# Kernel optimization log

Measured on AMD Instinct MI355X. Metric: run time of the kernel, lower is better.

Reference implementation:

```python
import jax, jax.numpy as jnp
import numpy as np

B, S, C, NH, DH, MH = 2, 2304, 1280, 8, 160, 64
SR = 48  # int(sqrt(S)); S = SR*SR
FMAX = jnp.finfo(jnp.float32).max


def _h2b(x):
    # diffusers head_to_batch_dim: [b,s,c] -> [b*heads, s, dh] (batch-major)
    b, s, c = x.shape
    return x.reshape(b, s, NH, DH).transpose(0, 2, 1, 3).reshape(b * NH, s, DH)


def _b2h(x):
    # diffusers batch_to_head_dim: [b*heads, s, dh] -> [b, s, c]
    bh, s, d = x.shape
    b = bh // NH
    return x.reshape(b, NH, s, d).transpose(0, 2, 1, 3).reshape(b, s, NH * d)


def _nearest(x, out):
    # torch F.interpolate(mode='nearest') on [b,1,h,w] square input -> [b,1,out,out]
    h, w = x.shape[-2], x.shape[-1]
    ih = jnp.arange(out) * h // out
    iw = jnp.arange(out) * w // out
    return x[:, :, ih, :][:, :, :, iw]


def setup_inputs():
    key = jax.random.key(0)
    ks = jax.random.split(key, 10)
    return {
        "hidden_states": jax.random.normal(ks[0], (B, S, C), jnp.float32),
        "Wq": jax.random.normal(ks[1], (C, C), jnp.float32) * 0.02,
        "Wk": jax.random.normal(ks[2], (C, C), jnp.float32) * 0.02,
        "Wv": jax.random.normal(ks[3], (C, C), jnp.float32) * 0.02,
        "Wo": jax.random.normal(ks[4], (C, C), jnp.float32) * 0.02,
        "bo": jnp.zeros((C,), jnp.float32),
        "store_ks": jax.random.normal(ks[5], (B * NH, S, DH), jnp.float32),
        "store_vs": jax.random.normal(ks[6], (B * NH, S, DH), jnp.float32),
        "mask_id": jax.random.bernoulli(ks[7], 0.5, (B, 1, MH, MH)),
        "mask_ig": jax.random.uniform(ks[8], (B, 1, MH, MH), jnp.float32),
        "scale_learnable": jnp.full((1,), 0.5, jnp.float32),
    }


def reference(hidden_states, Wq, Wk, Wv, Wo, bo, store_ks, store_vs, mask_id, mask_ig, scale_learnable):
    inv = 1.0 / jnp.sqrt(jnp.float32(DH))
    # self-attention (attention_mask is None for the self path)
    q = _h2b(hidden_states @ Wq)   # [B*NH, S, DH]
    k = _h2b(hidden_states @ Wk)
    v = _h2b(hidden_states @ Wv)
    probs = jax.nn.softmax(jnp.einsum('bqd,bkd->bqk', q, k) * inv, axis=-1)
    hs = _b2h(probs @ v)  # [B, S, C]
    # IP-adapter reference attention with interpolated additive mask
    mask_f = jnp.where(mask_id, jnp.float32(1.0), -FMAX)          # masked_fill(mask==False, -max)
    mask_r = _nearest(mask_f, SR).reshape(B, 1, SR * SR)          # [B,1,S], broadcast over query rows
    mask_bh = jnp.tile(mask_r, (NH, 1, 1))                        # torch .repeat(8,1,1) tiling order
    scores_ref = jnp.einsum('bqd,bkd->bqk', q, store_ks) * inv + mask_bh
    probs_ref = jax.nn.softmax(scores_ref, axis=-1)
    hs_ref = _b2h(probs_ref @ store_vs)                           # [B, S, C]
    # masked, learnable-scaled residual combine (self.scale = 1.0 python float)
    mask_ig_r = _nearest(mask_ig, SR).reshape(B, SR * SR, 1)      # 'b c h w -> b (h w) c'
    out = hs + 1.0 * hs_ref * mask_ig_r * scale_learnable
    # to_out[0] linear + to_out[1] dropout (identity at eval)
    return out @ Wo + bo
```

## Files before the change

### kernel.cpp

```cpp
#include <hip/hip_runtime.h>


typedef unsigned short u16;
typedef unsigned int   u32;
typedef unsigned char  u8;
typedef __attribute__((ext_vector_type(8))) short bf16x8;
typedef __attribute__((ext_vector_type(4))) float f32x4;

#define MFMA16(a,b,c) __builtin_amdgcn_mfma_f32_16x16x32_bf16((a),(b),(c),0,0,0)

__device__ __forceinline__ u16 f2b(float f) {
  u32 u = __float_as_uint(f);
  return (u16)((u + 0x7fffu + ((u >> 16) & 1u)) >> 16);
}
__device__ __forceinline__ float b2f(u16 v) { return __uint_as_float(((u32)v) << 16); }

__global__ __launch_bounds__(256) void maskdet(const u32* __restrict__ mid, u32* mode)
{
  __shared__ int a0, a1, a2, a3;
  int tid = threadIdx.x;
  if (tid == 0) { a0 = 1; a1 = 1; a2 = 1; a3 = 0; }
  __syncthreads();
  #pragma unroll
  for (int j = 0; j < 4; j++) {
    u32 w = mid[tid*4 + j];
    if (w > 1u)                      atomicAnd(&a0, 0);
    if (w & 0xFEFEFEFEu)             atomicAnd(&a1, 0);
    if (w != 0u && w != 0x3F800000u) atomicAnd(&a2, 0);
    if ((w & 0xFFFFu) == 0x3F80u)    atomicOr(&a3, 1);
  }
  __syncthreads();
  if (tid == 0) mode[0] = a0 ? 0u : (a1 ? 1u : (a3 ? 2u : (a2 ? 3u : 0u)));
}

__global__ void maskprep(const void* mid, const float* __restrict__ mig_in,
                         float* __restrict__ mk, float* __restrict__ mg, const u32* mode)
{
  int j = blockIdx.x*256 + threadIdx.x;
  if (j >= 2*2304) return;
  u32 md = mode[0];
  int b = j / 2304, s = j % 2304;
  int i = s / 48, jj = s % 48;
  int ih = (i*4)/3, iw = (jj*4)/3;
  int src = b*4096 + ih*64 + iw;
  bool on;
  if      (md == 0) on = ((const int*)mid)[src] != 0;
  else if (md == 1) on = ((const u8*)mid)[src]  != 0;
  else if (md == 2) on = ((const u16*)mid)[src] != 0;
  else              on = ((const float*)mid)[src] != 0.0f;
  mk[j] = on ? 1.0f : 0.0f;
  mg[j] = mig_in[src];
}

__global__ __launch_bounds__(256) void transpose_w(
    const float* __restrict__ W0, const float* __restrict__ W1,
    const float* __restrict__ W2, const float* __restrict__ W3, u16* __restrict__ WT)
{
  __shared__ u16 t[32][33];
  int z = blockIdx.z;
  const float* s = (z==0)?W0:(z==1)?W1:(z==2)?W2:W3;
  u16* d = WT + (size_t)z*1280*1280;
  int tx = threadIdx.x & 31, ty = (threadIdx.x >> 5) * 4;
  int x = blockIdx.x*32 + tx;
  int y = blockIdx.y*32 + ty;
  #pragma unroll
  for (int i=0;i<4;i++) t[ty+i][tx] = f2b(s[(size_t)(y+i)*1280 + x]);
  __syncthreads();
  int x2 = blockIdx.y*32 + tx, y2 = blockIdx.x*32 + ty;
  #pragma unroll
  for (int i=0;i<4;i++) d[(size_t)(y2+i)*1280 + x2] = t[tx][ty+i];
}

__global__ __launch_bounds__(256) void conv(const float* __restrict__ src, u16* __restrict__ dst, int n)
{
  for (int i = blockIdx.x*256 + threadIdx.x; i < n; i += gridDim.x*256)
    dst[i] = f2b(src[i]);
}

__global__ __launch_bounds__(256) void transpose_vs(const float* __restrict__ src, u16* __restrict__ dst)
{
  __shared__ u16 t[32][33];
  int z = blockIdx.z;
  u16* d = dst + (size_t)z*160*2304;
  int tx = threadIdx.x & 31, ty = (threadIdx.x >> 5) * 4;
  int r0 = blockIdx.x*32, c0 = blockIdx.y*32;
  #pragma unroll
  for (int i=0;i<4;i++)
    t[ty+i][tx] = f2b(src[((size_t)z*2304 + r0+ty+i)*160 + c0+tx]);
  __syncthreads();
  #pragma unroll
  for (int i=0;i<4;i++) d[(size_t)(c0+ty+i)*2304 + r0+tx] = t[tx][ty+i];
}

__global__ __launch_bounds__(256, 2) void gemm128(
    const u16* __restrict__ A, const u16* __restrict__ BT,
    u16* __restrict__ dq, u16* __restrict__ dk, u16* __restrict__ dvt,
    float* __restrict__ dout, const float* __restrict__ bias, int kind)
{
  __shared__ __align__(16) u16 As[128*40];
  __shared__ __align__(16) u16 Bs[128*40];
  int tid = threadIdx.x;
  int m0 = blockIdx.x*128, n0 = blockIdx.y*128;
  int z = blockIdx.z;
  const u16* Bt = BT + (size_t)z*1280*1280;
  int w = tid>>6, lane = tid&63, quad = lane>>4, l16 = lane&15;
  int wm = w&1, wn = w>>1;
  int arow = tid>>1, acg = (tid&1)*16;
  f32x4 zero = {0.f,0.f,0.f,0.f};
  f32x4 acc[4][4];
  #pragma unroll
  for (int a=0;a<4;a++) { acc[a][0]=zero; acc[a][1]=zero; acc[a][2]=zero; acc[a][3]=zero; }
  const u16* ga = A  + (size_t)(m0+arow)*1280 + acg;
  const u16* gb = Bt + (size_t)(n0+arow)*1280 + acg;
  for (int k0 = 0; k0 < 1280; k0 += 32) {
    uint4 a0 = *(const uint4*)(ga + k0);
    uint4 a1 = *(const uint4*)(ga + k0 + 8);
    uint4 b0 = *(const uint4*)(gb + k0);
    uint4 b1 = *(const uint4*)(gb + k0 + 8);
    __syncthreads();
    *(uint4*)&As[arow*40 + acg]     = a0;
    *(uint4*)&As[arow*40 + acg + 8] = a1;
    *(uint4*)&Bs[arow*40 + acg]     = b0;
    *(uint4*)&Bs[arow*40 + acg + 8] = b1;
    __syncthreads();
    bf16x8 af[4], bfr[4];
    #pragma unroll
    for (int mt=0; mt<4; mt++) af[mt]  = *(const bf16x8*)&As[(wm*64+mt*16+l16)*40 + quad*8];
    #pragma unroll
    for (int nt=0; nt<4; nt++) bfr[nt] = *(const bf16x8*)&Bs[(wn*64+nt*16+l16)*40 + quad*8];
    #pragma unroll
    for (int mt=0; mt<4; mt++)
      #pragma unroll
      for (int nt=0; nt<4; nt++)
        acc[mt][nt] = MFMA16(af[mt], bfr[nt], acc[mt][nt]);
  }
  #pragma unroll
  for (int mt=0; mt<4; mt++) {
    int r0g = m0 + wm*64 + mt*16 + quad*4;
    #pragma unroll
    for (int nt=0; nt<4; nt++) {
      int col = n0 + wn*64 + nt*16 + l16;
      if (kind == 1) {
        float bi = bias[col];
        #pragma unroll
        for (int r=0;r<4;r++) dout[(size_t)(r0g+r)*1280 + col] = acc[mt][nt][r] + bi;
      } else {
        int h = col/160, d = col%160;
        if (z == 2) {
          int b = r0g/2304, s0 = r0g%2304;
          size_t base = ((size_t)((b*8+h)*160 + d))*2304 + s0;
          ushort4 pk;
          pk.x = f2b(acc[mt][nt][0]); pk.y = f2b(acc[mt][nt][1]);
          pk.z = f2b(acc[mt][nt][2]); pk.w = f2b(acc[mt][nt][3]);
          *(ushort4*)&dvt[base] = pk;
        } else {
          u16* dst = (z==0)? dq : dk;
          #pragma unroll
          for (int r=0;r<4;r++) {
            int rg = r0g + r;
            int b = rg/2304, s = rg%2304;
            dst[((size_t)(b*8+h)*2304 + s)*160 + d] = f2b(acc[mt][nt][r]);
          }
        }
      }
    }
  }
}

__global__ __launch_bounds__(256, 2) void attn(
    const u16* __restrict__ qg,
    const u16* __restrict__ kg,
    const u16* __restrict__ vtg,
    const float* __restrict__ maskkey, const float* __restrict__ mig,
    u16* __restrict__ hs, u16* __restrict__ comb,
    const void* scaleptr, int ip)
{
  __shared__ __align__(16) u16 Ks[64*168];
  __shared__ __align__(16) u16 Ps[4*16*72];
  int bh = blockIdx.y, qt = blockIdx.x;
  int tid = threadIdx.x, w = tid>>6, lane = tid&63, quad = lane>>4, l16 = lane&15;
  int q0 = qt*64 + w*16;
  const float inv = 0.07905694150420949f;

  bf16x8 aq[5];
  {
    const u16* qrow = qg + ((size_t)bh*2304 + q0 + l16)*160 + quad*8;
    #pragma unroll
    for (int ks=0; ks<5; ks++) aq[ks] = *(const bf16x8*)(qrow + ks*32);
  }
  f32x4 zero = {0.f,0.f,0.f,0.f};
  f32x4 o[10];
  #pragma unroll
  for (int i=0;i<10;i++) o[i] = zero;
  float mrun[4] = {-1e30f,-1e30f,-1e30f,-1e30f};
  float lrun[4] = {0.f,0.f,0.f,0.f};

  int krow = tid>>2, kcg = (tid&3)*40;
  const u16* kbase = kg + ((size_t)bh*2304 + krow)*160 + kcg;
  const u16* vbase = vtg + ((size_t)bh*160 + l16)*2304 + quad*8;

  for (int kc = 0; kc < 36; kc++) {
    uint4 kv[5];
    #pragma unroll
    for (int i=0;i<5;i++) kv[i] = *(const uint4*)(kbase + (size_t)kc*64*160 + i*8);
    __syncthreads();
    #pragma unroll
    for (int i=0;i<5;i++) *(uint4*)&Ks[krow*168 + kcg + i*8] = kv[i];
    __syncthreads();

    f32x4 sc[4];
    bool keep[4];
    #pragma unroll
    for (int nt=0; nt<4; nt++) {
      f32x4 s = zero;
      #pragma unroll
      for (int ks=0; ks<5; ks++) {
        bf16x8 bk = *(const bf16x8*)&Ks[(nt*16+l16)*168 + ks*32 + quad*8];
        s = MFMA16(aq[ks], bk, s);
      }
      #pragma unroll
      for (int r=0;r<4;r++) s[r] *= inv;
      keep[nt] = true;
      if (ip) {
        int key = kc*64 + nt*16 + l16;
        if (maskkey[(bh & 1)*2304 + key] == 0.0f) {
          keep[nt] = false;
          #pragma unroll
          for (int r=0;r<4;r++) s[r] = -1e30f;
        }
      }
      sc[nt] = s;
    }

    float p[4][4];
    #pragma unroll
    for (int r=0;r<4;r++) {
      float mrow = fmaxf(fmaxf(sc[0][r], sc[1][r]), fmaxf(sc[2][r], sc[3][r]));
      #pragma unroll
      for (int off=1; off<16; off<<=1) mrow = fmaxf(mrow, __shfl_xor(mrow, off));
      float nm = fmaxf(mrun[r], mrow);
      float alpha = __expf(fminf(mrun[r] - nm, 0.f));
      mrun[r] = nm;
      float rs = 0.f;
      #pragma unroll
      for (int nt=0;nt<4;nt++) {
        float e = keep[nt] ? __expf(sc[nt][r] - nm) : 0.f;
        p[nt][r] = e; rs += e;
      }
      #pragma unroll
      for (int off=1; off<16; off<<=1) rs += __shfl_xor(rs, off);
      lrun[r] = lrun[r]*alpha + rs;
      #pragma unroll
      for (int nt2=0; nt2<10; nt2++) o[nt2][r] *= alpha;
    }

    #pragma unroll
    for (int nt=0;nt<4;nt++)
      #pragma unroll
      for (int r=0;r<4;r++)
        Ps[(w*16 + quad*4 + r)*72 + nt*16 + l16] = f2b(p[nt][r]);

    #pragma unroll
    for (int kb=0; kb<2; kb++) {
      bf16x8 ap = *(const bf16x8*)&Ps[(w*16 + l16)*72 + kb*32 + quad*8];
      #pragma unroll
      for (int nt=0; nt<10; nt++) {
        bf16x8 bv = *(const bf16x8*)(vbase + (size_t)nt*16*2304 + kc*64 + kb*32);
        o[nt] = MFMA16(ap, bv, o[nt]);
      }
    }
  }

  int b = bh>>3, h = bh&7;
  float scl = 0.f;
  if (ip) {
    u16 v0 = ((const u16*)scaleptr)[0];
    int e = (v0 >> 7) & 0xFF;
    scl = (v0 != 0 && e >= 100 && e <= 133) ? b2f(v0) : ((const float*)scaleptr)[0];
  }
  #pragma unroll
  for (int r=0;r<4;r++) {
    int s = q0 + quad*4 + r;
    float linv = (lrun[r] > 0.f) ? 1.0f/lrun[r] : 0.f;
    size_t base = ((size_t)b*2304 + s)*1280 + h*160;
    if (!ip) {
      #pragma unroll
      for (int nt=0;nt<10;nt++) hs[base + nt*16 + l16] = f2b(o[nt][r]*linv);
    } else {
      float f = mig[b*2304 + s]*scl*linv;
      #pragma unroll
      for (int nt=0;nt<10;nt++)
        comb[base + nt*16 + l16] = f2b(b2f(hs[base + nt*16 + l16]) + o[nt][r]*f);
    }
  }
}

extern "C" void kernel_launch(void* const* d_in, const int* in_sizes, int n_in,
                              void* d_out, int out_size, void* d_ws, size_t ws_size,
                              hipStream_t stream)
{
  const float* hid = (const float*)d_in[0];
  const float* Wq  = (const float*)d_in[1];
  const float* Wk  = (const float*)d_in[2];
  const float* Wv  = (const float*)d_in[3];
  const float* Wo  = (const float*)d_in[4];
  const float* bo  = (const float*)d_in[5];
  const float* sks = (const float*)d_in[6];
  const float* svs = (const float*)d_in[7];
  const void*  mid = d_in[8];
  const float* mig = (const float*)d_in[9];
  const void*  scl = d_in[10];

  char* ws = (char*)d_ws;
  float* mk   = (float*)(ws);
  float* mg   = (float*)(ws + 18432);
  u32*  mode  = (u32*)(ws + 36864);
  u16*  WT    = (u16*)(ws + 40960);
  u16*  hidB  = (u16*)(ws + 13148160);
  u16*  q     = (u16*)(ws + 24944640);
  u16*  kB    = (u16*)(ws + 36741120);
  u16*  vt    = (u16*)(ws + 48537600);
  u16*  hsB   = (u16*)(ws + 60334080);

  maskdet     <<<dim3(1),       256, 0, stream>>>((const u32*)mid, mode);
  maskprep    <<<dim3(18),      256, 0, stream>>>(mid, mig, mk, mg, mode);
  transpose_w <<<dim3(40,40,4), 256, 0, stream>>>(Wq, Wk, Wv, Wo, WT);
  conv        <<<dim3(2880),    256, 0, stream>>>(hid, hidB, 5898240);
  gemm128     <<<dim3(36,10,3), 256, 0, stream>>>(hidB, WT, q, kB, vt, nullptr, nullptr, 0);
  conv        <<<dim3(2880),    256, 0, stream>>>(sks, hidB, 5898240);
  attn        <<<dim3(36,16),   256, 0, stream>>>(q, kB, vt, nullptr, nullptr, hsB, nullptr, scl, 0);
  transpose_vs<<<dim3(72,5,16), 256, 0, stream>>>(svs, vt);
  attn        <<<dim3(36,16),   256, 0, stream>>>(q, hidB, vt, mk, mg, hsB, kB, scl, 1);
  gemm128     <<<dim3(36,10,1), 256, 0, stream>>>(kB, WT + (size_t)3*1280*1280,
                                                  nullptr, nullptr, nullptr, (float*)d_out, bo, 1);
}
```

Before: 1.071 ms.

## Pad K rows to LDS stride and load K tiles via direct global-to-LDS loads

K and stored keys are now written to global memory with a padded row stride of 168 elements, done by a new convK kernel and by the gemm epilogue. That lets each 64-row K tile be copied as one contiguous block straight into LDS with global_load_lds, skipping the trip through registers and the separate LDS stores. The goal is fewer VGPRs and less instruction overhead in the attention kernel's K staging. In exchange the K buffers and the conversion pass use about 5% more memory and bandwidth, and the workspace layout changes, which raises the risk of overlapping buffers.

New measurement: 958.1 us. -10.5%, faster.

```diff
diff --git a/kernel.cpp b/kernel.cpp
--- a/kernel.cpp
+++ b/kernel.cpp
@@ -8,6 +8,11 @@
 typedef __attribute__((ext_vector_type(4))) float f32x4;
 
 #define MFMA16(a,b,c) __builtin_amdgcn_mfma_f32_16x16x32_bf16((a),(b),(c),0,0,0)
+#define KPAD 168
+
+typedef const __attribute__((address_space(1))) void gvoid;
+typedef __attribute__((address_space(3))) void lvoid;
+#define GLD16(gp, lp) __builtin_amdgcn_global_load_lds((gvoid*)(gp), (lvoid*)(lp), 16, 0, 0)
 
 __device__ __forceinline__ u16 f2b(float f) {
   u32 u = __float_as_uint(f);
@@ -75,6 +80,15 @@
 {
   for (int i = blockIdx.x*256 + threadIdx.x; i < n; i += gridDim.x*256)
     dst[i] = f2b(src[i]);
+}
+
+__global__ __launch_bounds__(256) void convK(const float* __restrict__ src, u16* __restrict__ dst)
+{
+  const int n = 16*2304*KPAD;
+  for (int i = blockIdx.x*256 + threadIdx.x; i < n; i += gridDim.x*256) {
+    int row = i / KPAD, col = i % KPAD;
+    dst[i] = (col < 160) ? f2b(src[(size_t)row*160 + col]) : (u16)0;
+  }
 }
 
 __global__ __launch_bounds__(256) void transpose_vs(const float* __restrict__ src, u16* __restrict__ dst)
@@ -154,12 +168,12 @@
           pk.z = f2b(acc[mt][nt][2]); pk.w = f2b(acc[mt][nt][3]);
           *(ushort4*)&dvt[base] = pk;
         } else {
-          u16* dst = (z==0)? dq : dk;
           #pragma unroll
           for (int r=0;r<4;r++) {
             int rg = r0g + r;
             int b = rg/2304, s = rg%2304;
-            dst[((size_t)(b*8+h)*2304 + s)*160 + d] = f2b(acc[mt][nt][r]);
+            if (z == 0) dq[((size_t)(b*8+h)*2304 + s)*160  + d] = f2b(acc[mt][nt][r]);
+            else        dk[((size_t)(b*8+h)*2304 + s)*KPAD + d] = f2b(acc[mt][nt][r]);
           }
         }
       }
@@ -175,7 +189,7 @@
     u16* __restrict__ hs, u16* __restrict__ comb,
     const void* scaleptr, int ip)
 {
-  __shared__ __align__(16) u16 Ks[64*168];
+  __shared__ __align__(16) u16 Ks[64*KPAD];
   __shared__ __align__(16) u16 Ps[4*16*72];
   int bh = blockIdx.y, qt = blockIdx.x;
   int tid = threadIdx.x, w = tid>>6, lane = tid&63, quad = lane>>4, l16 = lane&15;
@@ -195,17 +209,20 @@
   float mrun[4] = {-1e30f,-1e30f,-1e30f,-1e30f};
   float lrun[4] = {0.f,0.f,0.f,0.f};
 
-  int krow = tid>>2, kcg = (tid&3)*40;
-  const u16* kbase = kg + ((size_t)bh*2304 + krow)*160 + kcg;
   const u16* vbase = vtg + ((size_t)bh*160 + l16)*2304 + quad*8;
+  const char* kgbytes = (const char*)kg;
 
   for (int kc = 0; kc < 36; kc++) {
-    uint4 kv[5];
-    #pragma unroll
-    for (int i=0;i<5;i++) kv[i] = *(const uint4*)(kbase + (size_t)kc*64*160 + i*8);
+    const char* tile = kgbytes + ((size_t)bh*2304 + (size_t)kc*64)*(KPAD*2);
     __syncthreads();
-    #pragma unroll
-    for (int i=0;i<5;i++) *(uint4*)&Ks[krow*168 + kcg + i*8] = kv[i];
+    {
+      int off = w*1024 + lane*16;
+      #pragma unroll
+      for (int j=0;j<5;j++)
+        GLD16(tile + j*4096 + off, (char*)Ks + j*4096 + w*1024);
+      if (w == 0)
+        GLD16(tile + 20480 + lane*16, (char*)Ks + 20480);
+    }
     __syncthreads();
 
     f32x4 sc[4];
@@ -215,7 +232,7 @@
       f32x4 s = zero;
       #pragma unroll
       for (int ks=0; ks<5; ks++) {
-        bf16x8 bk = *(const bf16x8*)&Ks[(nt*16+l16)*168 + ks*32 + quad*8];
+        bf16x8 bk = *(const bf16x8*)&Ks[(nt*16+l16)*KPAD + ks*32 + quad*8];
         s = MFMA16(aq[ks], bk, s);
       }
       #pragma unroll
@@ -316,21 +333,21 @@
   float* mg   = (float*)(ws + 18432);
   u32*  mode  = (u32*)(ws + 36864);
   u16*  WT    = (u16*)(ws + 40960);
-  u16*  hidB  = (u16*)(ws + 13148160);
-  u16*  q     = (u16*)(ws + 24944640);
-  u16*  kB    = (u16*)(ws + 36741120);
-  u16*  vt    = (u16*)(ws + 48537600);
-  u16*  hsB   = (u16*)(ws + 60334080);
+  u16*  slotA = (u16*)(ws + 13148160);
+  u16*  q     = (u16*)(ws + 25534464);
+  u16*  slotB = (u16*)(ws + 37330944);
+  u16*  vt    = (u16*)(ws + 49717248);
+  u16*  hsB   = (u16*)(ws + 61513728);
 
   maskdet     <<<dim3(1),       256, 0, stream>>>((const u32*)mid, mode);
   maskprep    <<<dim3(18),      256, 0, stream>>>(mid, mig, mk, mg, mode);
   transpose_w <<<dim3(40,40,4), 256, 0, stream>>>(Wq, Wk, Wv, Wo, WT);
-  conv        <<<dim3(2880),    256, 0, stream>>>(hid, hidB, 5898240);
-  gemm128     <<<dim3(36,10,3), 256, 0, stream>>>(hidB, WT, q, kB, vt, nullptr, nullptr, 0);
-  conv        <<<dim3(2880),    256, 0, stream>>>(sks, hidB, 5898240);
-  attn        <<<dim3(36,16),   256, 0, stream>>>(q, kB, vt, nullptr, nullptr, hsB, nullptr, scl, 0);
+  conv        <<<dim3(2880),    256, 0, stream>>>(hid, slotA, 5898240);
+  gemm128     <<<dim3(36,10,3), 256, 0, stream>>>(slotA, WT, q, slotB, vt, nullptr, nullptr, 0);
+  convK       <<<dim3(6048),    256, 0, stream>>>(sks, slotA);
+  attn        <<<dim3(36,16),   256, 0, stream>>>(q, slotB, vt, nullptr, nullptr, hsB, nullptr, scl, 0);
   transpose_vs<<<dim3(72,5,16), 256, 0, stream>>>(svs, vt);
-  attn        <<<dim3(36,16),   256, 0, stream>>>(q, hidB, vt, mk, mg, hsB, kB, scl, 1);
-  gemm128     <<<dim3(36,10,1), 256, 0, stream>>>(kB, WT + (size_t)3*1280*1280,
+  attn        <<<dim3(36,16),   256, 0, stream>>>(q, slotA, vt, mk, mg, hsB, slotB, scl, 1);
+  gemm128     <<<dim3(36,10,1), 256, 0, stream>>>(slotB, WT + (size_t)3*1280*1280,
                                                   nullptr, nullptr, nullptr, (float*)d_out, bo, 1);
 }
```
